# Kernel tuning notes

Hardware: AMD Instinct MI355X
Metric: run time of the kernel (lower is better)

The kernel has to match this reference:

```python
import jax, jax.numpy as jnp
import numpy as np

N, IN_DIM, HIDDEN, OUT_DIM, K = 16384, 64, 128, 128, 32


def setup_inputs() -> dict:
    key = jax.random.key(0)
    k1, k2, k3 = jax.random.split(key, 3)
    x = jax.random.normal(k1, (N, IN_DIM), dtype=jnp.float32)
    std1 = 1.0 / np.sqrt(2 * IN_DIM)
    w = jax.random.uniform(k2, (HIDDEN, 2 * IN_DIM), dtype=jnp.float32, minval=-std1, maxval=std1)
    std2 = 1.0 / np.sqrt(IN_DIM + HIDDEN)
    w2 = jax.random.uniform(k3, (OUT_DIM, IN_DIM + HIDDEN), dtype=jnp.float32, minval=-std2, maxval=std2)
    return {"x": x, "w": w, "w2": w2, "k": K}


def reference(x, w, w2, k):
    # kNN graph via squared euclidean distances (same ordering as torch.norm cdist)
    sq = jnp.sum(x * x, axis=-1)                      # (N,)
    d2 = sq[:, None] + sq[None, :] - 2.0 * (x @ x.T)  # (N, N)
    _, graph = jax.lax.top_k(-d2, k)                  # (N, k) indices of k smallest distances
    # gather neighbor features and concat broadcast self features
    nb = x[graph]                                      # (N, k, in_dim)
    self_rep = jnp.broadcast_to(x[:, None, :], nb.shape)
    feat = jnp.concatenate([nb, self_rep], axis=-1)    # (N, k, 2*in_dim)
    # linear + Hardtanh + average pooling over neighborhood
    h = jnp.clip(jnp.einsum('nkf,hf->nkh', feat, w), -1.0, 1.0)
    pooled = h.mean(axis=1)                            # (N, hidden)
    # second linear on [pooled, x]
    out = jnp.concatenate([pooled, x], axis=-1) @ w2.T # (N, out_dim)
    return out
```

## Files before the change

kernel.cpp:

```cpp
#include <hip/hip_runtime.h>

#define NPTS   16384
#define IN_DIM 64
#define HID    128
#define KSEL   32

#define CAP    96
#define TRIG   80
#define WIN_HI 48
#define SLACK  0.30f

typedef _Float16 f16x8 __attribute__((ext_vector_type(8)));
typedef float    f32x4 __attribute__((ext_vector_type(4)));
typedef unsigned short u16;
typedef unsigned int   u32;
typedef unsigned long long u64;

__global__ __launch_bounds__(256) void prep_kernel(const float* __restrict__ x,
                                                   float* __restrict__ sq,
                                                   u16* __restrict__ ph,
                                                   u16* __restrict__ pl) {
    const int i  = blockIdx.x * 256 + threadIdx.x;
    const int ct = i >> 4, li = i & 15;
    const float4* xr = (const float4*)(x + (size_t)i * IN_DIM);
    float s = 0.f;
#pragma unroll
    for (int c = 0; c < 8; ++c) {
        float4 a = xr[2 * c], b = xr[2 * c + 1];
        float e[8] = {a.x, a.y, a.z, a.w, b.x, b.y, b.z, b.w};
        u32 hw[8], lw[8];
#pragma unroll
        for (int j = 0; j < 8; ++j) {
            s += e[j] * e[j];
            _Float16 h = (_Float16)e[j];
            float hf = (float)h;
            _Float16 l = (_Float16)(e[j] - hf);
            hw[j] = __builtin_bit_cast(u16, h);
            lw[j] = __builtin_bit_cast(u16, l);
        }
        size_t off = ((size_t)ct * 8 + c) * 128 + (size_t)li * 8;
        *(uint4*)(ph + off) = make_uint4(hw[0] | (hw[1] << 16), hw[2] | (hw[3] << 16),
                                         hw[4] | (hw[5] << 16), hw[6] | (hw[7] << 16));
        *(uint4*)(pl + off) = make_uint4(lw[0] | (lw[1] << 16), lw[2] | (lw[3] << 16),
                                         lw[4] | (lw[5] << 16), lw[6] | (lw[7] << 16));
    }
    sq[i] = s;
}

__device__ __forceinline__ void compact_row(float* bdrow, u16* bjrow, int* pcnt,
                                            u32* pthr, int lane) {
    int n = *pcnt; n = n < CAP ? n : CAP;
    const float INF = __int_as_float(0x7f800000);
    float dv0 = (lane      < n) ? bdrow[lane]      : INF;
    float dv1 = (lane + 64 < n) ? bdrow[lane + 64] : INF;
    u16   jv0 = (lane      < n) ? bjrow[lane]      : 0;
    u16   jv1 = (lane + 64 < n) ? bjrow[lane + 64] : 0;
    u32 u0 = __float_as_uint(dv0), u1 = __float_as_uint(dv1);
    u32 lo = 0, hi = *pthr, ans = hi;
    for (int it = 0; it < 26 && lo < hi; ++it) {
        u32 mid = lo + ((hi - lo) >> 1);
        int c = __popcll(__ballot(u0 <= mid)) + __popcll(__ballot(u1 <= mid));
        if (c < 32) lo = mid + 1;
        else { hi = mid; ans = mid; if (c <= WIN_HI) break; }
    }
    float ansf = __uint_as_float(ans) + SLACK;
    u64 mlt = (1ull << lane) - 1ull;
    bool p0 = dv0 <= ansf;
    u64 b0 = __ballot(p0);
    if (p0) { int p = __popcll(b0 & mlt); bdrow[p] = dv0; bjrow[p] = jv0; }
    int base = __popcll(b0);
    bool p1 = dv1 <= ansf;
    u64 b1 = __ballot(p1);
    if (p1) { int p = base + __popcll(b1 & mlt); if (p < CAP) { bdrow[p] = dv1; bjrow[p] = jv1; } }
    base += __popcll(b1);
    if (lane == 0) {
        *pcnt = base < CAP ? base : CAP;
        atomicMin(pthr, __float_as_uint(ansf));
    }
}

__global__ __launch_bounds__(256, 4) void knn_kernel(const float* __restrict__ x,
                                                     const u16* __restrict__ ph,
                                                     const u16* __restrict__ pl,
                                                     const float* __restrict__ sq,
                                                     int* __restrict__ graph) {
    __shared__ float bd[4][16][CAP];
    __shared__ u16   bj[4][16][CAP];
    __shared__ int   bcnt[4][16];
    __shared__ u32   bthrU[16];

    const int t = threadIdx.x, lane = t & 63, wave = t >> 6;
    const int g = lane >> 4, li = lane & 15;
    const int rg = blockIdx.x;
    const int rbase = rg * 16;

    if (t < 64) bcnt[t >> 4][t & 15] = 0;
    if (t < 16) bthrU[t] = 0x7f800000u;

    f16x8 ah[2], al[2];
#pragma unroll
    for (int kh = 0; kh < 2; ++kh) {
        size_t o = ((size_t)rg * 2 + kh) * 512 + (size_t)lane * 8;
        ah[kh] = *(const f16x8*)(ph + o);
        al[kh] = *(const f16x8*)(pl + o);
    }
    float sar[4];
#pragma unroll
    for (int r = 0; r < 4; ++r) sar[r] = sq[rbase + g * 4 + r];
    __syncthreads();

    int ct = wave;
    f16x8 cb0 = *(const f16x8*)(ph + (size_t)ct * 1024 +       (size_t)lane * 8);
    f16x8 cb1 = *(const f16x8*)(ph + (size_t)ct * 1024 + 512 + (size_t)lane * 8);
    float csb = sq[ct * 16 + li];

    for (int i = 0; i < 256; ++i) {
        f16x8 nb0, nb1; float nsb = 0.f;
        const int nct = ct + 4;
        if (i < 255) {
            nb0 = *(const f16x8*)(ph + (size_t)nct * 1024 +       (size_t)lane * 8);
            nb1 = *(const f16x8*)(ph + (size_t)nct * 1024 + 512 + (size_t)lane * 8);
            nsb = sq[nct * 16 + li];
        }
        f32x4 acc = {0.f, 0.f, 0.f, 0.f};
        acc = __builtin_amdgcn_mfma_f32_16x16x32_f16(ah[0], cb0, acc, 0, 0, 0);
        acc = __builtin_amdgcn_mfma_f32_16x16x32_f16(ah[1], cb1, acc, 0, 0, 0);
        acc = __builtin_amdgcn_mfma_f32_16x16x32_f16(al[0], cb0, acc, 0, 0, 0);
        acc = __builtin_amdgcn_mfma_f32_16x16x32_f16(al[1], cb1, acc, 0, 0, 0);

        uint4 tu = *(const uint4*)&bthrU[g * 4];
        const float thr[4] = {__uint_as_float(tu.x), __uint_as_float(tu.y),
                              __uint_as_float(tu.z), __uint_as_float(tu.w)};
#pragma unroll
        for (int r = 0; r < 4; ++r) {
            float d = fmaf(-2.f, acc[r], sar[r] + csb);
            if (d <= thr[r]) {
                int row = g * 4 + r;
                int pos = atomicAdd(&bcnt[wave][row], 1);
                if (pos < CAP) {
                    bd[wave][row][pos] = fmaxf(d, 0.f);
                    bj[wave][row][pos] = (u16)(ct * 16 + li);
                }
            }
        }
        u64 need = __ballot((lane < 16) && (bcnt[wave][lane & 15] > TRIG));
        while (need) {
            int rr = __ffsll((long long)need) - 1;
            need &= need - 1;
            compact_row(bd[wave][rr], bj[wave][rr], &bcnt[wave][rr], &bthrU[rr], lane);
        }
        ct = nct; cb0 = nb0; cb1 = nb1; csb = nsb;
    }

    __syncthreads();

    const u64 mlt = (1ull << lane) - 1ull;
    for (int ii = 0; ii < 4; ++ii) {
        const int lr = wave * 4 + ii;
        const int gr = rbase + lr;
        const float sqa = sq[gr];
        const float4* xa = (const float4*)(x + (size_t)gr * IN_DIM);
        const int ns0 = min(bcnt[0][lr], CAP), ns1 = min(bcnt[1][lr], CAP);
        const int ns2 = min(bcnt[2][lr], CAP), ns3 = min(bcnt[3][lr], CAP);
        u32 db[6]; int jj[6];
#pragma unroll
        for (int s6 = 0; s6 < 6; ++s6) {
            int f = lane + s6 * 64;
            int sl = f / CAP, idx = f - sl * CAP;
            int nsl = sl == 0 ? ns0 : sl == 1 ? ns1 : sl == 2 ? ns2 : ns3;
            u32 dbits = 0x7f800000u; int j = 0;
            if (idx < nsl) {
                j = bj[sl][lr][idx];
                const float4* xb = (const float4*)(x + (size_t)j * IN_DIM);
                float dot = 0.f;
#pragma unroll
                for (int q = 0; q < 16; ++q) {
                    float4 a = xa[q], b = xb[q];
                    dot += a.x * b.x + a.y * b.y + a.z * b.z + a.w * b.w;
                }
                float d = fmaxf(fmaf(-2.f, dot, sqa + sq[j]), 0.f);
                dbits = __float_as_uint(d);
            }
            db[s6] = dbits; jj[s6] = j;
        }
        u32 lo = 0, hi = 0x7f800000u, ans = hi;
        for (int it = 0; it < 32 && lo < hi; ++it) {
            u32 mid = lo + ((hi - lo) >> 1);
            int c = 0;
#pragma unroll
            for (int s6 = 0; s6 < 6; ++s6)
                c += __popcll(__ballot(db[s6] <= mid));
            if (c < 32) lo = mid + 1;
            else { hi = mid; ans = mid; if (c == 32) break; }
        }
        bool tie[6]; int c_lt = 0, c_le = 0;
#pragma unroll
        for (int s6 = 0; s6 < 6; ++s6) {
            tie[s6] = (db[s6] == ans);
            c_lt += __popcll(__ballot(db[s6] < ans));
            c_le += __popcll(__ballot(db[s6] <= ans));
        }
        int extra = (c_le - c_lt) - (32 - c_lt);
        while (extra > 0) {
            int mx = -1;
#pragma unroll
            for (int s6 = 0; s6 < 6; ++s6) if (tie[s6] && jj[s6] > mx) mx = jj[s6];
#pragma unroll
            for (int off = 32; off > 0; off >>= 1) {
                int o = __shfl_xor(mx, off); mx = mx > o ? mx : o;
            }
#pragma unroll
            for (int s6 = 0; s6 < 6; ++s6) if (tie[s6] && jj[s6] == mx) tie[s6] = false;
            --extra;
        }
        int* gp = graph + (size_t)gr * KSEL;
        int base = 0;
#pragma unroll
        for (int s6 = 0; s6 < 6; ++s6) {
            bool k = (db[s6] < ans) || tie[s6];
            u64 b = __ballot(k);
            if (k) gp[base + __popcll(b & mlt)] = jj[s6];
            base += __popcll(b);
        }
    }
}

__global__ __launch_bounds__(384) void xw_kernel(const float* __restrict__ x,
                                                 const float* __restrict__ w,
                                                 const float* __restrict__ w2,
                                                 float* __restrict__ XWa,
                                                 float* __restrict__ XWb,
                                                 float* __restrict__ outb) {
    __shared__ float xs[64][64];
    const int t = threadIdx.x;
    const int rbase = blockIdx.x * 64;

    for (int idx = t; idx < 64 * 16; idx += 384) {
        int r = idx >> 4, q = idx & 15;
        ((float4*)xs[r])[q] = ((const float4*)(x + (size_t)(rbase + r) * IN_DIM))[q];
    }
    const int kind = t >> 7;
    const int idx  = t & 127;
    const float* wp = (kind == 0) ? (w + (size_t)idx * 128)
                    : (kind == 1) ? (w + (size_t)idx * 128 + 64)
                                  : (w2 + (size_t)idx * 192 + 128);
    float4 wreg[16];
#pragma unroll
    for (int q = 0; q < 16; ++q) wreg[q] = ((const float4*)wp)[q];
    __syncthreads();

    for (int r = 0; r < 64; ++r) {
        float acc = 0.f;
#pragma unroll
        for (int q = 0; q < 16; ++q) {
            float4 xv = ((float4*)xs[r])[q];
            acc += xv.x * wreg[q].x + xv.y * wreg[q].y +
                   xv.z * wreg[q].z + xv.w * wreg[q].w;
        }
        size_t o = (size_t)(rbase + r) * 128 + idx;
        if (kind == 0)      XWa[o]  = acc;
        else if (kind == 1) XWb[o]  = acc;
        else                outb[o] = acc;
    }
}

__global__ __launch_bounds__(256) void pool_kernel(const int* __restrict__ graph,
                                                   const float* __restrict__ XWa,
                                                   const float* __restrict__ XWb,
                                                   float* __restrict__ pooled) {
    const int t = threadIdx.x, lane = t & 63, wave = t >> 6;
    const int row = blockIdx.x * 4 + wave;
    int gi = graph[(size_t)row * KSEL + (lane & 31)];
    float2 b = ((const float2*)(XWb + (size_t)row * HID))[lane];
    float2 acc = {0.f, 0.f};
#pragma unroll
    for (int c = 0; c < KSEL; ++c) {
        int j = __shfl(gi, c);
        float2 v = ((const float2*)(XWa + (size_t)j * HID))[lane];
        acc.x += fminf(fmaxf(v.x + b.x, -1.f), 1.f);
        acc.y += fminf(fmaxf(v.y + b.y, -1.f), 1.f);
    }
    float2* pr = (float2*)(pooled + (size_t)row * HID);
    pr[lane] = make_float2(acc.x * (1.f / 32.f), acc.y * (1.f / 32.f));
}

__global__ __launch_bounds__(256) void out_kernel(const float* __restrict__ pooled,
                                                  const float* __restrict__ w2,
                                                  float* __restrict__ out) {
    __shared__ float ws2[128][132];
    __shared__ float pt[64][128];
    const int t = threadIdx.x;
    const int rbase = blockIdx.x * 64;

    for (int idx = t; idx < 128 * 32; idx += 256) {
        int o = idx >> 5, q = idx & 31;
        ((float4*)&ws2[o][0])[q] = ((const float4*)(w2 + (size_t)o * 192))[q];
    }
    for (int idx = t; idx < 64 * 32; idx += 256) {
        int r = idx >> 5, q = idx & 31;
        ((float4*)&pt[r][0])[q] = ((const float4*)(pooled + (size_t)(rbase + r) * 128))[q];
    }
    __syncthreads();

    const int o = t & 127, rsub = t >> 7;
    for (int rp = 0; rp < 32; ++rp) {
        int r = rp * 2 + rsub;
        float acc = 0.f;
#pragma unroll
        for (int q = 0; q < 32; ++q) {
            float4 pv = ((float4*)&pt[r][0])[q];
            float4 wv = ((float4*)&ws2[o][0])[q];
            acc += pv.x * wv.x + pv.y * wv.y + pv.z * wv.z + pv.w * wv.w;
        }
        size_t off = (size_t)(rbase + r) * 128 + o;
        out[off] += acc;
    }
}

extern "C" void kernel_launch(void* const* d_in, const int* in_sizes, int n_in,
                              void* d_out, int out_size, void* d_ws, size_t ws_size,
                              hipStream_t stream) {
    const float* x  = (const float*)d_in[0];
    const float* w  = (const float*)d_in[1];
    const float* w2 = (const float*)d_in[2];
    float* out = (float*)d_out;

    float* sq     = (float*)d_ws;
    int*   graph  = (int*)(sq + NPTS);
    float* XWa    = (float*)(graph + (size_t)NPTS * KSEL);
    float* XWb    = XWa + (size_t)NPTS * HID;
    float* region = XWb + (size_t)NPTS * HID;
    u16*   ph     = (u16*)region;
    u16*   pl     = ph + (size_t)NPTS * IN_DIM;
    float* pooled = region;

    prep_kernel<<<NPTS / 256, 256, 0, stream>>>(x, sq, ph, pl);
    knn_kernel<<<NPTS / 16, 256, 0, stream>>>(x, ph, pl, sq, graph);
    xw_kernel<<<NPTS / 64, 384, 0, stream>>>(x, w, w2, XWa, XWb, out);
    pool_kernel<<<NPTS / 4, 256, 0, stream>>>(graph, XWa, XWb, pooled);
    out_kernel<<<NPTS / 64, 256, 0, stream>>>(pooled, w2, out);
}
```

Baseline: 622.5 us.

## Process four column tiles per kNN iteration with wider candidate buffers

The kNN scan loop now handles four 16-column tiles per iteration, issuing 16 MFMAs and prefetching four tiles ahead. This cuts loop overhead and the number of threshold checks and compaction checks per tile. A wave-level __any guard skips the atomic insert path when no lane qualifies. The candidate buffer capacity grows to 128 and the compaction trigger drops to 64, and the final select now covers 8 slots of 64. In exchange, register pressure rises, the occupancy hint drops from 4 to 3, and shared memory use grows.

```diff
diff --git a/kernel.cpp b/kernel.cpp
--- a/kernel.cpp
+++ b/kernel.cpp
@@ -5,10 +5,11 @@
 #define HID    128
 #define KSEL   32
 
-#define CAP    96
-#define TRIG   80
+#define CAP    128
+#define TRIG   64
 #define WIN_HI 48
 #define SLACK  0.30f
+#define INFBITS 0x7f800000u
 
 typedef _Float16 f16x8 __attribute__((ext_vector_type(8)));
 typedef float    f32x4 __attribute__((ext_vector_type(4)));
@@ -50,7 +51,7 @@
 __device__ __forceinline__ void compact_row(float* bdrow, u16* bjrow, int* pcnt,
                                             u32* pthr, int lane) {
     int n = *pcnt; n = n < CAP ? n : CAP;
-    const float INF = __int_as_float(0x7f800000);
+    const float INF = __int_as_float(INFBITS);
     float dv0 = (lane      < n) ? bdrow[lane]      : INF;
     float dv1 = (lane + 64 < n) ? bdrow[lane + 64] : INF;
     u16   jv0 = (lane      < n) ? bjrow[lane]      : 0;
@@ -79,7 +80,7 @@
     }
 }
 
-__global__ __launch_bounds__(256, 4) void knn_kernel(const float* __restrict__ x,
+__global__ __launch_bounds__(256, 3) void knn_kernel(const float* __restrict__ x,
                                                      const u16* __restrict__ ph,
                                                      const u16* __restrict__ pl,
                                                      const float* __restrict__ sq,
@@ -95,7 +96,7 @@
     const int rbase = rg * 16;
 
     if (t < 64) bcnt[t >> 4][t & 15] = 0;
-    if (t < 16) bthrU[t] = 0x7f800000u;
+    if (t < 16) bthrU[t] = INFBITS;
 
     f16x8 ah[2], al[2];
 #pragma unroll
@@ -109,47 +110,68 @@
     for (int r = 0; r < 4; ++r) sar[r] = sq[rbase + g * 4 + r];
     __syncthreads();
 
-    int ct = wave;
-    f16x8 cb0 = *(const f16x8*)(ph + (size_t)ct * 1024 +       (size_t)lane * 8);
-    f16x8 cb1 = *(const f16x8*)(ph + (size_t)ct * 1024 + 512 + (size_t)lane * 8);
-    float csb = sq[ct * 16 + li];
-
-    for (int i = 0; i < 256; ++i) {
-        f16x8 nb0, nb1; float nsb = 0.f;
-        const int nct = ct + 4;
-        if (i < 255) {
-            nb0 = *(const f16x8*)(ph + (size_t)nct * 1024 +       (size_t)lane * 8);
-            nb1 = *(const f16x8*)(ph + (size_t)nct * 1024 + 512 + (size_t)lane * 8);
-            nsb = sq[nct * 16 + li];
-        }
-        f32x4 acc = {0.f, 0.f, 0.f, 0.f};
-        acc = __builtin_amdgcn_mfma_f32_16x16x32_f16(ah[0], cb0, acc, 0, 0, 0);
-        acc = __builtin_amdgcn_mfma_f32_16x16x32_f16(ah[1], cb1, acc, 0, 0, 0);
-        acc = __builtin_amdgcn_mfma_f32_16x16x32_f16(al[0], cb0, acc, 0, 0, 0);
-        acc = __builtin_amdgcn_mfma_f32_16x16x32_f16(al[1], cb1, acc, 0, 0, 0);
-
+    int ctb = wave * 4;
+    f16x8 cb[4][2]; float csb[4];
+#pragma unroll
+    for (int c = 0; c < 4; ++c) {
+        size_t o = (size_t)(ctb + c) * 1024 + (size_t)lane * 8;
+        cb[c][0] = *(const f16x8*)(ph + o);
+        cb[c][1] = *(const f16x8*)(ph + o + 512);
+        csb[c] = sq[(ctb + c) * 16 + li];
+    }
+
+    for (int i = 0; i < 64; ++i) {
+        const int nctb = ctb + 16;
+        f16x8 nb[4][2]; float nsb[4];
+        if (i < 63) {
+#pragma unroll
+            for (int c = 0; c < 4; ++c) {
+                size_t o = (size_t)(nctb + c) * 1024 + (size_t)lane * 8;
+                nb[c][0] = *(const f16x8*)(ph + o);
+                nb[c][1] = *(const f16x8*)(ph + o + 512);
+                nsb[c] = sq[(nctb + c) * 16 + li];
+            }
+        }
+        f32x4 acc[4];
+#pragma unroll
+        for (int c = 0; c < 4; ++c) {
+            f32x4 a = {0.f, 0.f, 0.f, 0.f};
+            a = __builtin_amdgcn_mfma_f32_16x16x32_f16(ah[0], cb[c][0], a, 0, 0, 0);
+            a = __builtin_amdgcn_mfma_f32_16x16x32_f16(ah[1], cb[c][1], a, 0, 0, 0);
+            a = __builtin_amdgcn_mfma_f32_16x16x32_f16(al[0], cb[c][0], a, 0, 0, 0);
+            a = __builtin_amdgcn_mfma_f32_16x16x32_f16(al[1], cb[c][1], a, 0, 0, 0);
+            acc[c] = a;
+        }
         uint4 tu = *(const uint4*)&bthrU[g * 4];
         const float thr[4] = {__uint_as_float(tu.x), __uint_as_float(tu.y),
                               __uint_as_float(tu.z), __uint_as_float(tu.w)};
 #pragma unroll
-        for (int r = 0; r < 4; ++r) {
-            float d = fmaf(-2.f, acc[r], sar[r] + csb);
-            if (d <= thr[r]) {
-                int row = g * 4 + r;
-                int pos = atomicAdd(&bcnt[wave][row], 1);
-                if (pos < CAP) {
-                    bd[wave][row][pos] = fmaxf(d, 0.f);
-                    bj[wave][row][pos] = (u16)(ct * 16 + li);
+        for (int c = 0; c < 4; ++c) {
+#pragma unroll
+            for (int r = 0; r < 4; ++r) {
+                float d = fmaf(-2.f, acc[c][r], sar[r] + csb[c]);
+                bool pred = d <= thr[r];
+                if (__any(pred)) {
+                    if (pred) {
+                        int row = g * 4 + r;
+                        int pos = atomicAdd(&bcnt[wave][row], 1);
+                        if (pos < CAP) {
+                            bd[wave][row][pos] = fmaxf(d, 0.f);
+                            bj[wave][row][pos] = (u16)((ctb + c) * 16 + li);
+                        }
+                    }
                 }
             }
         }
-        u64 need = __ballot((lane < 16) && (bcnt[wave][lane & 15] > TRIG));
+        u64 need = __ballot((lane < 16) && (bcnt[wave][lane] > TRIG));
         while (need) {
             int rr = __ffsll((long long)need) - 1;
             need &= need - 1;
             compact_row(bd[wave][rr], bj[wave][rr], &bcnt[wave][rr], &bthrU[rr], lane);
         }
-        ct = nct; cb0 = nb0; cb1 = nb1; csb = nsb;
+        ctb = nctb;
+#pragma unroll
+        for (int c = 0; c < 4; ++c) { cb[c][0] = nb[c][0]; cb[c][1] = nb[c][1]; csb[c] = nsb[c]; }
     }
 
     __syncthreads();
@@ -160,66 +182,68 @@
         const int gr = rbase + lr;
         const float sqa = sq[gr];
         const float4* xa = (const float4*)(x + (size_t)gr * IN_DIM);
-        const int ns0 = min(bcnt[0][lr], CAP), ns1 = min(bcnt[1][lr], CAP);
-        const int ns2 = min(bcnt[2][lr], CAP), ns3 = min(bcnt[3][lr], CAP);
-        u32 db[6]; int jj[6];
-#pragma unroll
-        for (int s6 = 0; s6 < 6; ++s6) {
-            int f = lane + s6 * 64;
-            int sl = f / CAP, idx = f - sl * CAP;
-            int nsl = sl == 0 ? ns0 : sl == 1 ? ns1 : sl == 2 ? ns2 : ns3;
-            u32 dbits = 0x7f800000u; int j = 0;
-            if (idx < nsl) {
-                j = bj[sl][lr][idx];
-                const float4* xb = (const float4*)(x + (size_t)j * IN_DIM);
-                float dot = 0.f;
-#pragma unroll
-                for (int q = 0; q < 16; ++q) {
-                    float4 a = xa[q], b = xb[q];
-                    dot += a.x * b.x + a.y * b.y + a.z * b.z + a.w * b.w;
+        int ns[4];
+#pragma unroll
+        for (int s = 0; s < 4; ++s) { int v = bcnt[s][lr]; ns[s] = v < CAP ? v : CAP; }
+        u32 db[8]; int jj[8];
+#pragma unroll
+        for (int s8 = 0; s8 < 8; ++s8) {
+            const int sl = s8 >> 1;
+            const int half = s8 & 1;
+            u32 dbits = INFBITS; int j = 0;
+            if (ns[sl] > half * 64) {
+                int idx = half * 64 + lane;
+                if (idx < ns[sl]) {
+                    j = bj[sl][lr][idx];
+                    const float4* xb = (const float4*)(x + (size_t)j * IN_DIM);
+                    float dot = 0.f;
+#pragma unroll
+                    for (int q = 0; q < 16; ++q) {
+                        float4 a = xa[q], b = xb[q];
+                        dot += a.x * b.x + a.y * b.y + a.z * b.z + a.w * b.w;
+                    }
+                    float d = fmaxf(fmaf(-2.f, dot, sqa + sq[j]), 0.f);
+                    dbits = __float_as_uint(d);
                 }
-                float d = fmaxf(fmaf(-2.f, dot, sqa + sq[j]), 0.f);
-                dbits = __float_as_uint(d);
             }
-            db[s6] = dbits; jj[s6] = j;
-        }
-        u32 lo = 0, hi = 0x7f800000u, ans = hi;
+            db[s8] = dbits; jj[s8] = j;
+        }
+        u32 lo = 0, hi = INFBITS, ans = hi;
         for (int it = 0; it < 32 && lo < hi; ++it) {
             u32 mid = lo + ((hi - lo) >> 1);
             int c = 0;
 #pragma unroll
-            for (int s6 = 0; s6 < 6; ++s6)
-                c += __popcll(__ballot(db[s6] <= mid));
+            for (int s8 = 0; s8 < 8; ++s8)
+                c += __popcll(__ballot(db[s8] <= mid));
             if (c < 32) lo = mid + 1;
             else { hi = mid; ans = mid; if (c == 32) break; }
         }
-        bool tie[6]; int c_lt = 0, c_le = 0;
-#pragma unroll
-        for (int s6 = 0; s6 < 6; ++s6) {
-            tie[s6] = (db[s6] == ans);
-            c_lt += __popcll(__ballot(db[s6] < ans));
-            c_le += __popcll(__ballot(db[s6] <= ans));
-        }
-        int extra = (c_le - c_lt) - (32 - c_lt);
+        bool tie[8]; int c_le = 0;
+#pragma unroll
+        for (int s8 = 0; s8 < 8; ++s8) {
+            tie[s8] = (db[s8] == ans);
+            c_le += __popcll(__ballot(db[s8] <= ans));
+        }
+        int extra = c_le - 32;
         while (extra > 0) {
             int mx = -1;
 #pragma unroll
-            for (int s6 = 0; s6 < 6; ++s6) if (tie[s6] && jj[s6] > mx) mx = jj[s6];
+            for (int s8 = 0; s8 < 8; ++s8) if (tie[s8] && jj[s8] > mx) mx = jj[s8];
 #pragma unroll
             for (int off = 32; off > 0; off >>= 1) {
                 int o = __shfl_xor(mx, off); mx = mx > o ? mx : o;
             }
 #pragma unroll
-            for (int s6 = 0; s6 < 6; ++s6) if (tie[s6] && jj[s6] == mx) tie[s6] = false;
+            for (int s8 = 0; s8 < 8; ++s8) if (tie[s8] && jj[s8] == mx) tie[s8] = false;
             --extra;
         }
         int* gp = graph + (size_t)gr * KSEL;
         int base = 0;
 #pragma unroll
-        for (int s6 = 0; s6 < 6; ++s6) {
-            bool k = (db[s6] < ans) || tie[s6];
+        for (int s8 = 0; s8 < 8; ++s8) {
+            bool k = (db[s8] < ans) || tie[s8];
             u64 b = __ballot(k);
-            if (k) gp[base + __popcll(b & mlt)] = jj[s6];
+            if (k) gp[base + __popcll(b & mlt)] = jj[s8];
             base += __popcll(b);
         }
     }
```

After: 767.6 us. 1.23x slower.
